# Kernel optimization log

Hardware: AMD Instinct MI355X
Metric: run time of the kernel (lower is better)

The kernel has to match this reference:

```python
import jax, jax.numpy as jnp
import numpy as np

N_NODES = 100000
N_EDGES = 3200000
D_FEAT = 128
HIDDEN = 16
N_CLASSES = 8


def setup_inputs() -> dict:
    key = jax.random.key(0)
    k1, k2, k3, k4 = jax.random.split(key, 4)
    x = jax.random.normal(k1, (N_NODES, D_FEAT), dtype=jnp.float32)
    edge_index = jax.random.randint(k2, (2, N_EDGES), 0, N_NODES, dtype=jnp.int64)
    W1 = jax.random.normal(k3, (D_FEAT, HIDDEN), dtype=jnp.float32) * (1.0 / np.sqrt(D_FEAT))
    b1 = jnp.zeros((HIDDEN,), dtype=jnp.float32)
    W2 = jax.random.normal(k4, (HIDDEN, N_CLASSES), dtype=jnp.float32) * (1.0 / np.sqrt(HIDDEN))
    b2 = jnp.zeros((N_CLASSES,), dtype=jnp.float32)
    return {"x": x, "edge_index": edge_index, "W1": W1, "b1": b1, "W2": W2, "b2": b2}


def _gcn_conv(x, W, b, src, dst, deg_inv_sqrt, n_nodes):
    h = x @ W  # [N, F_out]
    norm = deg_inv_sqrt[src] * deg_inv_sqrt[dst]  # [E']
    msg = h[src] * norm[:, None]  # gather + scale
    out = jax.ops.segment_sum(msg, dst, num_segments=n_nodes)  # scatter-add
    return out + b


def _prep_edges(edge_index, n_nodes):
    # add self-loops (PyG GCNConv default) and compute symmetric norm degrees
    loop = jnp.arange(n_nodes, dtype=edge_index.dtype)
    src = jnp.concatenate([edge_index[0], loop])
    dst = jnp.concatenate([edge_index[1], loop])
    deg = jax.ops.segment_sum(jnp.ones_like(dst, dtype=jnp.float32), dst,
                              num_segments=n_nodes)
    deg_inv_sqrt = jnp.where(deg > 0, jax.lax.rsqrt(jnp.maximum(deg, 1.0)), 0.0)
    return src, dst, deg_inv_sqrt


def reference(x, edge_index, W1, b1, W2, b2):
    n_nodes = x.shape[0]
    src, dst, deg_inv_sqrt = _prep_edges(edge_index, n_nodes)
    h = jax.nn.relu(_gcn_conv(x, W1, b1, src, dst, deg_inv_sqrt, n_nodes))
    logits = _gcn_conv(h, W2, b2, src, dst, deg_inv_sqrt, n_nodes)
    return jax.nn.log_softmax(logits, axis=1)
```

## Files before the change

### kernel.cpp

```cpp
#include <hip/hip_runtime.h>

#define N_NODES 100000
#define N_EDGES 3200000
#define D_FEAT 128
#define HIDDEN 16
#define NCLS 8

#define NBKT 256
#define BSZ  391
#define CHUNK 8192
#define NCHUNK 391
#define TOTH (NBKT * NCHUNK)
#define NBS1 (TOTH / 256)


__global__ __launch_bounds__(256) void k_hist(const int* __restrict__ dst,
                                              unsigned* __restrict__ hist) {
    __shared__ unsigned h[NBKT];
    int tid = threadIdx.x;
    h[tid] = 0u;
    __syncthreads();
    int base = blockIdx.x * CHUNK;
    #pragma unroll
    for (int it = 0; it < CHUNK / 256; ++it) {
        int e = base + it * 256 + tid;
        if (e < N_EDGES) atomicAdd(&h[dst[e] / BSZ], 1u);
    }
    __syncthreads();
    hist[(unsigned)tid * NCHUNK + blockIdx.x] = h[tid];
}

__global__ void k_scan1(unsigned* __restrict__ a, unsigned* __restrict__ bsum) {
    __shared__ unsigned s[256];
    int tid = threadIdx.x;
    int i = blockIdx.x * 256 + tid;
    unsigned v = a[i];
    s[tid] = v; __syncthreads();
    for (int off = 1; off < 256; off <<= 1) {
        unsigned t = (tid >= off) ? s[tid - off] : 0u;
        __syncthreads();
        s[tid] += t;
        __syncthreads();
    }
    a[i] = s[tid] - v;
    if (tid == 255) bsum[blockIdx.x] = s[255];
}

__global__ void k_scan2(unsigned* __restrict__ bsum) {
    __shared__ unsigned s[512];
    int tid = threadIdx.x;
    unsigned v = (tid < NBS1) ? bsum[tid] : 0u;
    s[tid] = v; __syncthreads();
    for (int off = 1; off < 512; off <<= 1) {
        unsigned t = (tid >= off) ? s[tid - off] : 0u;
        __syncthreads();
        s[tid] += t;
        __syncthreads();
    }
    bsum[tid] = s[tid] - v;
}

__global__ void k_scan3(unsigned* __restrict__ a, const unsigned* __restrict__ bsum) {
    int i = blockIdx.x * blockDim.x + threadIdx.x;
    a[i] += bsum[i >> 8];
}

__global__ __launch_bounds__(256) void k_fill(const int* __restrict__ src,
                                              const int* __restrict__ dst,
                                              const unsigned* __restrict__ hist,
                                              unsigned* __restrict__ rec) {
    __shared__ unsigned cur[NBKT];
    int tid = threadIdx.x;
    cur[tid] = hist[(unsigned)tid * NCHUNK + blockIdx.x];
    __syncthreads();
    int base = blockIdx.x * CHUNK;
    #pragma unroll
    for (int it = 0; it < CHUNK / 256; ++it) {
        int e = base + it * 256 + tid;
        if (e < N_EDGES) {
            int d = dst[e];
            int b = d / BSZ;
            unsigned p = atomicAdd(&cur[b], 1u);
            rec[p] = ((unsigned)src[e] << 9) | (unsigned)(d - b * BSZ);
        }
    }
}

__global__ __launch_bounds__(1024) void k_dis2(const unsigned* __restrict__ hist,
                                               const unsigned* __restrict__ rec,
                                               float* __restrict__ dis) {
    __shared__ unsigned cnt[BSZ];
    int tid = threadIdx.x;
    int bkt = blockIdx.x;
    int node0 = bkt * BSZ;
    int nn = (node0 + BSZ <= N_NODES) ? BSZ : (N_NODES - node0);
    for (int n = tid; n < nn; n += 1024) cnt[n] = 1u;
    __syncthreads();
    unsigned start = hist[(unsigned)bkt * NCHUNK];
    unsigned end = (bkt == NBKT - 1) ? N_EDGES : hist[(unsigned)(bkt + 1) * NCHUNK];
    for (unsigned e = start + tid; e < end; e += 1024)
        atomicAdd(&cnt[rec[e] & 511u], 1u);
    __syncthreads();
    for (int n = tid; n < nn; n += 1024)
        dis[node0 + n] = rsqrtf((float)cnt[n]);
}

__global__ __launch_bounds__(256) void k_gemm1(const float* __restrict__ x,
                                               const float* __restrict__ W1,
                                               const float* __restrict__ dis,
                                               float* __restrict__ hd1) {
    __shared__ float sW[D_FEAT * HIDDEN];
    __shared__ float sx[64][132];
    int tid = threadIdx.x;
    for (int t = tid; t < D_FEAT * HIDDEN; t += 256) sW[t] = W1[t];

    int node0 = blockIdx.x * 64;
    #pragma unroll
    for (int it = 0; it < 8; ++it) {
        int lin = it * 256 + tid;
        int r   = lin >> 5;
        int c4  = lin & 31;
        int row = node0 + r;
        float4 v = make_float4(0.f, 0.f, 0.f, 0.f);
        if (row < N_NODES)
            v = *(const float4*)(x + (size_t)row * D_FEAT + c4 * 4);
        *(float4*)(&sx[r][c4 * 4]) = v;
    }
    __syncthreads();

    int lr   = tid >> 2;
    int node = node0 + lr;
    int f0   = (tid & 3) * 4;
    if (node >= N_NODES) return;

    float a0 = 0.f, a1 = 0.f, a2 = 0.f, a3 = 0.f;
    #pragma unroll
    for (int k = 0; k < D_FEAT; ++k) {
        float xv = sx[lr][k];
        a0 += xv * sW[k * HIDDEN + f0 + 0];
        a1 += xv * sW[k * HIDDEN + f0 + 1];
        a2 += xv * sW[k * HIDDEN + f0 + 2];
        a3 += xv * sW[k * HIDDEN + f0 + 3];
    }
    float s = dis[node];
    *(float4*)(hd1 + (size_t)node * HIDDEN + f0) = make_float4(a0 * s, a1 * s, a2 * s, a3 * s);
}

__global__ __launch_bounds__(1024) void k_aggB(const unsigned* __restrict__ hist,
                                               const unsigned* __restrict__ rec,
                                               const float* __restrict__ hd1,
                                               const float* __restrict__ dis,
                                               const float* __restrict__ b1,
                                               const float* __restrict__ W2,
                                               float* __restrict__ hd2) {
    __shared__ float acc[BSZ][HIDDEN + 1];
    __shared__ float sW2[HIDDEN * NCLS];
    __shared__ float sb1[HIDDEN];
    int tid = threadIdx.x;
    int bkt = blockIdx.x;
    int node0 = bkt * BSZ;
    int nn = (node0 + BSZ <= N_NODES) ? BSZ : (N_NODES - node0);
    if (tid < HIDDEN * NCLS) sW2[tid] = W2[tid];
    if (tid < HIDDEN)        sb1[tid] = b1[tid];

    int j = tid & 15, rr = tid >> 4;
    for (int r = rr; r < nn; r += 64)
        acc[r][j] = hd1[(size_t)(node0 + r) * HIDDEN + j];
    __syncthreads();

    unsigned start = hist[(unsigned)bkt * NCHUNK];
    unsigned end = (bkt == NBKT - 1) ? N_EDGES : hist[(unsigned)(bkt + 1) * NCHUNK];
    for (unsigned e = start + rr; e < end; e += 64) {
        unsigned r = rec[e];
        unsigned s = r >> 9, dl = r & 511u;
        float v = hd1[(size_t)s * HIDDEN + j];
        atomicAdd(&acc[dl][j], v);
    }
    __syncthreads();

    for (int n = tid; n < nn; n += 1024) {
        int node = node0 + n;
        float dv = dis[node];
        float hbuf[HIDDEN];
        #pragma unroll
        for (int m = 0; m < HIDDEN; ++m)
            hbuf[m] = fmaxf(dv * acc[n][m] + sb1[m], 0.f);
        float o[NCLS];
        #pragma unroll
        for (int k = 0; k < NCLS; ++k) {
            float t = 0.f;
            #pragma unroll
            for (int m = 0; m < HIDDEN; ++m) t += hbuf[m] * sW2[m * NCLS + k];
            o[k] = dv * t;
        }
        float4* hp = (float4*)(hd2 + (size_t)node * NCLS);
        hp[0] = make_float4(o[0], o[1], o[2], o[3]);
        hp[1] = make_float4(o[4], o[5], o[6], o[7]);
    }
}

__global__ __launch_bounds__(1024) void k_aggC(const unsigned* __restrict__ hist,
                                               const unsigned* __restrict__ rec,
                                               const float* __restrict__ hd2,
                                               const float* __restrict__ dis,
                                               const float* __restrict__ b2,
                                               float* __restrict__ out) {
    __shared__ float acc[BSZ][NCLS + 1];
    int tid = threadIdx.x;
    int bkt = blockIdx.x;
    int node0 = bkt * BSZ;
    int nn = (node0 + BSZ <= N_NODES) ? BSZ : (N_NODES - node0);

    int j = tid & 7, rr = tid >> 3;
    for (int r = rr; r < nn; r += 128)
        acc[r][j] = hd2[(size_t)(node0 + r) * NCLS + j];
    __syncthreads();

    unsigned start = hist[(unsigned)bkt * NCHUNK];
    unsigned end = (bkt == NBKT - 1) ? N_EDGES : hist[(unsigned)(bkt + 1) * NCHUNK];
    for (unsigned e = start + rr; e < end; e += 128) {
        unsigned r = rec[e];
        unsigned s = r >> 9, dl = r & 511u;
        atomicAdd(&acc[dl][j], hd2[(size_t)s * NCLS + j]);
    }
    __syncthreads();

    for (int n = tid; n < nn; n += 1024) {
        int node = node0 + n;
        float dv = dis[node];
        float l[NCLS];
        float m = -1e30f;
        #pragma unroll
        for (int k = 0; k < NCLS; ++k) {
            l[k] = dv * acc[n][k] + b2[k];
            m = fmaxf(m, l[k]);
        }
        float ssum = 0.f;
        #pragma unroll
        for (int k = 0; k < NCLS; ++k) ssum += __expf(l[k] - m);
        float lse = logf(ssum) + m;
        float4* op = (float4*)(out + (size_t)node * NCLS);
        op[0] = make_float4(l[0] - lse, l[1] - lse, l[2] - lse, l[3] - lse);
        op[1] = make_float4(l[4] - lse, l[5] - lse, l[6] - lse, l[7] - lse);
    }
}

extern "C" void kernel_launch(void* const* d_in, const int* in_sizes, int n_in,
                              void* d_out, int out_size, void* d_ws, size_t ws_size,
                              hipStream_t stream) {
    const float* x  = (const float*)d_in[0];
    const int*   ei = (const int*)d_in[1];
    const float* W1 = (const float*)d_in[2];
    const float* b1 = (const float*)d_in[3];
    const float* W2 = (const float*)d_in[4];
    const float* b2 = (const float*)d_in[5];
    float* out = (float*)d_out;

    const int* src = ei;
    const int* dst = ei + N_EDGES;

    unsigned* ws = (unsigned*)d_ws;
    const size_t N = N_NODES;
    float*    dis  = (float*)ws;
    unsigned* hist = ws + N;
    unsigned* bsum = hist + TOTH;
    unsigned* rec  = bsum + 512;
    float*    hd1  = (float*)(rec + N_EDGES);
    float*    hd2  = hd1 + 16 * N;

    k_hist <<<NCHUNK, 256, 0, stream>>>(dst, hist);
    k_scan1<<<NBS1, 256, 0, stream>>>(hist, bsum);
    k_scan2<<<1, 512, 0, stream>>>(bsum);
    k_scan3<<<NBS1, 256, 0, stream>>>(hist, bsum);
    k_fill <<<NCHUNK, 256, 0, stream>>>(src, dst, hist, rec);
    k_dis2 <<<NBKT, 1024, 0, stream>>>(hist, rec, dis);
    k_gemm1<<<(N_NODES + 63) / 64, 256, 0, stream>>>(x, W1, dis, hd1);
    k_aggB <<<NBKT, 1024, 0, stream>>>(hist, rec, hd1, dis, b1, W2, hd2);
    k_aggC <<<NBKT, 1024, 0, stream>>>(hist, rec, hd2, dis, b2, out);
}
```

Before: 597.9 us.

## Split buckets finer and slice edges across blocks with global atomic merge

Doubles the bucket count to 512 with smaller buckets and splits each bucket's edge range across four 256-thread blocks, giving 2048 blocks instead of 256 to raise occupancy on the many CUs. Each slice accumulates partial sums in shared memory and merges them into global buffers with atomics. The per-node epilogues (ReLU plus second GEMM, and log_softmax) become separate node-parallel kernels, and the gather loops are unrolled by four to keep more loads in flight. The cost is extra kernel launches, global atomic traffic, additional buffer writes, and float summation order that is no longer deterministic.

```diff
diff --git a/kernel.cpp b/kernel.cpp
--- a/kernel.cpp
+++ b/kernel.cpp
@@ -6,19 +6,25 @@
 #define HIDDEN 16
 #define NCLS 8
 
-#define NBKT 256
-#define BSZ  391
+#define NBKT 512
+#define BSZ  196
+#define NSLICE 4
 #define CHUNK 8192
 #define NCHUNK 391
 #define TOTH (NBKT * NCHUNK)
 #define NBS1 (TOTH / 256)
 
 
+__global__ void k_zero_deg(unsigned* __restrict__ deg) {
+    int i = blockIdx.x * blockDim.x + threadIdx.x;
+    if (i < N_NODES) deg[i] = 0u;
+}
+
 __global__ __launch_bounds__(256) void k_hist(const int* __restrict__ dst,
                                               unsigned* __restrict__ hist) {
     __shared__ unsigned h[NBKT];
     int tid = threadIdx.x;
-    h[tid] = 0u;
+    h[tid] = 0u; h[tid + 256] = 0u;
     __syncthreads();
     int base = blockIdx.x * CHUNK;
     #pragma unroll
@@ -28,6 +34,7 @@
     }
     __syncthreads();
     hist[(unsigned)tid * NCHUNK + blockIdx.x] = h[tid];
+    hist[(unsigned)(tid + 256) * NCHUNK + blockIdx.x] = h[tid + 256];
 }
 
 __global__ void k_scan1(unsigned* __restrict__ a, unsigned* __restrict__ bsum) {
@@ -47,11 +54,11 @@
 }
 
 __global__ void k_scan2(unsigned* __restrict__ bsum) {
-    __shared__ unsigned s[512];
+    __shared__ unsigned s[1024];
     int tid = threadIdx.x;
     unsigned v = (tid < NBS1) ? bsum[tid] : 0u;
     s[tid] = v; __syncthreads();
-    for (int off = 1; off < 512; off <<= 1) {
+    for (int off = 1; off < 1024; off <<= 1) {
         unsigned t = (tid >= off) ? s[tid - off] : 0u;
         __syncthreads();
         s[tid] += t;
@@ -71,7 +78,8 @@
                                               unsigned* __restrict__ rec) {
     __shared__ unsigned cur[NBKT];
     int tid = threadIdx.x;
-    cur[tid] = hist[(unsigned)tid * NCHUNK + blockIdx.x];
+    cur[tid]       = hist[(unsigned)tid * NCHUNK + blockIdx.x];
+    cur[tid + 256] = hist[(unsigned)(tid + 256) * NCHUNK + blockIdx.x];
     __syncthreads();
     int base = blockIdx.x * CHUNK;
     #pragma unroll
@@ -81,34 +89,41 @@
             int d = dst[e];
             int b = d / BSZ;
             unsigned p = atomicAdd(&cur[b], 1u);
-            rec[p] = ((unsigned)src[e] << 9) | (unsigned)(d - b * BSZ);
+            rec[p] = ((unsigned)src[e] << 8) | (unsigned)(d - b * BSZ);
         }
     }
 }
 
-__global__ __launch_bounds__(1024) void k_dis2(const unsigned* __restrict__ hist,
-                                               const unsigned* __restrict__ rec,
-                                               float* __restrict__ dis) {
+__global__ __launch_bounds__(256) void k_deg(const unsigned* __restrict__ hist,
+                                             const unsigned* __restrict__ rec,
+                                             unsigned* __restrict__ deg) {
     __shared__ unsigned cnt[BSZ];
     int tid = threadIdx.x;
-    int bkt = blockIdx.x;
+    int bkt = blockIdx.x >> 2, slice = blockIdx.x & 3;
     int node0 = bkt * BSZ;
-    int nn = (node0 + BSZ <= N_NODES) ? BSZ : (N_NODES - node0);
-    for (int n = tid; n < nn; n += 1024) cnt[n] = 1u;
+    int nn = N_NODES - node0; if (nn > BSZ) nn = BSZ;
+    if (nn <= 0) return;
+    for (int n = tid; n < nn; n += 256) cnt[n] = 0u;
     __syncthreads();
     unsigned start = hist[(unsigned)bkt * NCHUNK];
     unsigned end = (bkt == NBKT - 1) ? N_EDGES : hist[(unsigned)(bkt + 1) * NCHUNK];
-    for (unsigned e = start + tid; e < end; e += 1024)
-        atomicAdd(&cnt[rec[e] & 511u], 1u);
-    __syncthreads();
-    for (int n = tid; n < nn; n += 1024)
-        dis[node0 + n] = rsqrtf((float)cnt[n]);
+    for (unsigned e = start + slice * 256 + tid; e < end; e += 1024)
+        atomicAdd(&cnt[rec[e] & 255u], 1u);
+    __syncthreads();
+    for (int n = tid; n < nn; n += 256)
+        if (cnt[n]) atomicAdd(&deg[node0 + n], cnt[n]);
+}
+
+__global__ void k_disk(const unsigned* __restrict__ deg, float* __restrict__ dis) {
+    int i = blockIdx.x * blockDim.x + threadIdx.x;
+    if (i < N_NODES) dis[i] = rsqrtf((float)(deg[i] + 1u));
 }
 
 __global__ __launch_bounds__(256) void k_gemm1(const float* __restrict__ x,
                                                const float* __restrict__ W1,
                                                const float* __restrict__ dis,
-                                               float* __restrict__ hd1) {
+                                               float* __restrict__ hd1,
+                                               float* __restrict__ agg1) {
     __shared__ float sW[D_FEAT * HIDDEN];
     __shared__ float sx[64][132];
     int tid = threadIdx.x;
@@ -143,106 +158,153 @@
         a3 += xv * sW[k * HIDDEN + f0 + 3];
     }
     float s = dis[node];
-    *(float4*)(hd1 + (size_t)node * HIDDEN + f0) = make_float4(a0 * s, a1 * s, a2 * s, a3 * s);
-}
-
-__global__ __launch_bounds__(1024) void k_aggB(const unsigned* __restrict__ hist,
-                                               const unsigned* __restrict__ rec,
-                                               const float* __restrict__ hd1,
-                                               const float* __restrict__ dis,
-                                               const float* __restrict__ b1,
-                                               const float* __restrict__ W2,
-                                               float* __restrict__ hd2) {
+    float4 o = make_float4(a0 * s, a1 * s, a2 * s, a3 * s);
+    *(float4*)(hd1  + (size_t)node * HIDDEN + f0) = o;
+    *(float4*)(agg1 + (size_t)node * HIDDEN + f0) = o;
+}
+
+__global__ __launch_bounds__(256) void k_agg1(const unsigned* __restrict__ hist,
+                                              const unsigned* __restrict__ rec,
+                                              const float* __restrict__ hd1,
+                                              float* __restrict__ agg1) {
     __shared__ float acc[BSZ][HIDDEN + 1];
+    int tid = threadIdx.x;
+    int bkt = blockIdx.x >> 2, slice = blockIdx.x & 3;
+    int node0 = bkt * BSZ;
+    int nn = N_NODES - node0; if (nn > BSZ) nn = BSZ;
+    if (nn <= 0) return;
+    for (int t = tid; t < nn * HIDDEN; t += 256) acc[t >> 4][t & 15] = 0.f;
+    __syncthreads();
+
+    unsigned start = hist[(unsigned)bkt * NCHUNK];
+    unsigned end = (bkt == NBKT - 1) ? N_EDGES : hist[(unsigned)(bkt + 1) * NCHUNK];
+    int j = tid & 15, rr = tid >> 4;
+    unsigned e = start + (unsigned)(slice * 16 + rr);
+    for (; e + 192u < end; e += 256u) {
+        unsigned r0 = rec[e], r1 = rec[e + 64u], r2 = rec[e + 128u], r3 = rec[e + 192u];
+        float v0 = hd1[(size_t)(r0 >> 8) * HIDDEN + j];
+        float v1 = hd1[(size_t)(r1 >> 8) * HIDDEN + j];
+        float v2 = hd1[(size_t)(r2 >> 8) * HIDDEN + j];
+        float v3 = hd1[(size_t)(r3 >> 8) * HIDDEN + j];
+        atomicAdd(&acc[r0 & 255u][j], v0);
+        atomicAdd(&acc[r1 & 255u][j], v1);
+        atomicAdd(&acc[r2 & 255u][j], v2);
+        atomicAdd(&acc[r3 & 255u][j], v3);
+    }
+    for (; e < end; e += 64u) {
+        unsigned r = rec[e];
+        atomicAdd(&acc[r & 255u][j], hd1[(size_t)(r >> 8) * HIDDEN + j]);
+    }
+    __syncthreads();
+    for (int t = tid; t < nn * HIDDEN; t += 256) {
+        float v = acc[t >> 4][t & 15];
+        if (v != 0.f) atomicAdd(&agg1[(size_t)node0 * HIDDEN + t], v);
+    }
+}
+
+__global__ __launch_bounds__(256) void k_epi1(const float* __restrict__ agg1,
+                                              const float* __restrict__ dis,
+                                              const float* __restrict__ b1,
+                                              const float* __restrict__ W2,
+                                              float* __restrict__ hd2,
+                                              float* __restrict__ agg2) {
     __shared__ float sW2[HIDDEN * NCLS];
     __shared__ float sb1[HIDDEN];
     int tid = threadIdx.x;
-    int bkt = blockIdx.x;
-    int node0 = bkt * BSZ;
-    int nn = (node0 + BSZ <= N_NODES) ? BSZ : (N_NODES - node0);
     if (tid < HIDDEN * NCLS) sW2[tid] = W2[tid];
     if (tid < HIDDEN)        sb1[tid] = b1[tid];
-
-    int j = tid & 15, rr = tid >> 4;
-    for (int r = rr; r < nn; r += 64)
-        acc[r][j] = hd1[(size_t)(node0 + r) * HIDDEN + j];
+    __syncthreads();
+    int i = blockIdx.x * 256 + tid;
+    if (i >= N_NODES) return;
+    float dv = dis[i];
+    float h[HIDDEN];
+    const float4* ap = (const float4*)(agg1 + (size_t)i * HIDDEN);
+    #pragma unroll
+    for (int q = 0; q < 4; ++q) {
+        float4 a = ap[q];
+        h[q * 4 + 0] = fmaxf(dv * a.x + sb1[q * 4 + 0], 0.f);
+        h[q * 4 + 1] = fmaxf(dv * a.y + sb1[q * 4 + 1], 0.f);
+        h[q * 4 + 2] = fmaxf(dv * a.z + sb1[q * 4 + 2], 0.f);
+        h[q * 4 + 3] = fmaxf(dv * a.w + sb1[q * 4 + 3], 0.f);
+    }
+    float o[NCLS];
+    #pragma unroll
+    for (int k = 0; k < NCLS; ++k) o[k] = 0.f;
+    #pragma unroll
+    for (int m = 0; m < HIDDEN; ++m) {
+        float hv = h[m];
+        #pragma unroll
+        for (int k = 0; k < NCLS; ++k) o[k] += hv * sW2[m * NCLS + k];
+    }
+    float4 o0 = make_float4(dv * o[0], dv * o[1], dv * o[2], dv * o[3]);
+    float4 o1 = make_float4(dv * o[4], dv * o[5], dv * o[6], dv * o[7]);
+    ((float4*)(hd2  + (size_t)i * NCLS))[0] = o0;
+    ((float4*)(hd2  + (size_t)i * NCLS))[1] = o1;
+    ((float4*)(agg2 + (size_t)i * NCLS))[0] = o0;
+    ((float4*)(agg2 + (size_t)i * NCLS))[1] = o1;
+}
+
+__global__ __launch_bounds__(256) void k_agg2(const unsigned* __restrict__ hist,
+                                              const unsigned* __restrict__ rec,
+                                              const float* __restrict__ hd2,
+                                              float* __restrict__ agg2) {
+    __shared__ float acc[BSZ][NCLS + 1];
+    int tid = threadIdx.x;
+    int bkt = blockIdx.x >> 2, slice = blockIdx.x & 3;
+    int node0 = bkt * BSZ;
+    int nn = N_NODES - node0; if (nn > BSZ) nn = BSZ;
+    if (nn <= 0) return;
+    for (int t = tid; t < nn * NCLS; t += 256) acc[t >> 3][t & 7] = 0.f;
     __syncthreads();
 
     unsigned start = hist[(unsigned)bkt * NCHUNK];
     unsigned end = (bkt == NBKT - 1) ? N_EDGES : hist[(unsigned)(bkt + 1) * NCHUNK];
-    for (unsigned e = start + rr; e < end; e += 64) {
+    int j = tid & 7, rr = tid >> 3;
+    unsigned e = start + (unsigned)(slice * 32 + rr);
+    for (; e + 384u < end; e += 512u) {
+        unsigned r0 = rec[e], r1 = rec[e + 128u], r2 = rec[e + 256u], r3 = rec[e + 384u];
+        float v0 = hd2[(size_t)(r0 >> 8) * NCLS + j];
+        float v1 = hd2[(size_t)(r1 >> 8) * NCLS + j];
+        float v2 = hd2[(size_t)(r2 >> 8) * NCLS + j];
+        float v3 = hd2[(size_t)(r3 >> 8) * NCLS + j];
+        atomicAdd(&acc[r0 & 255u][j], v0);
+        atomicAdd(&acc[r1 & 255u][j], v1);
+        atomicAdd(&acc[r2 & 255u][j], v2);
+        atomicAdd(&acc[r3 & 255u][j], v3);
+    }
+    for (; e < end; e += 128u) {
         unsigned r = rec[e];
-        unsigned s = r >> 9, dl = r & 511u;
-        float v = hd1[(size_t)s * HIDDEN + j];
-        atomicAdd(&acc[dl][j], v);
-    }
-    __syncthreads();
-
-    for (int n = tid; n < nn; n += 1024) {
-        int node = node0 + n;
-        float dv = dis[node];
-        float hbuf[HIDDEN];
-        #pragma unroll
-        for (int m = 0; m < HIDDEN; ++m)
-            hbuf[m] = fmaxf(dv * acc[n][m] + sb1[m], 0.f);
-        float o[NCLS];
-        #pragma unroll
-        for (int k = 0; k < NCLS; ++k) {
-            float t = 0.f;
-            #pragma unroll
-            for (int m = 0; m < HIDDEN; ++m) t += hbuf[m] * sW2[m * NCLS + k];
-            o[k] = dv * t;
-        }
-        float4* hp = (float4*)(hd2 + (size_t)node * NCLS);
-        hp[0] = make_float4(o[0], o[1], o[2], o[3]);
-        hp[1] = make_float4(o[4], o[5], o[6], o[7]);
-    }
-}
-
-__global__ __launch_bounds__(1024) void k_aggC(const unsigned* __restrict__ hist,
-                                               const unsigned* __restrict__ rec,
-                                               const float* __restrict__ hd2,
-                                               const float* __restrict__ dis,
-                                               const float* __restrict__ b2,
-                                               float* __restrict__ out) {
-    __shared__ float acc[BSZ][NCLS + 1];
-    int tid = threadIdx.x;
-    int bkt = blockIdx.x;
-    int node0 = bkt * BSZ;
-    int nn = (node0 + BSZ <= N_NODES) ? BSZ : (N_NODES - node0);
-
-    int j = tid & 7, rr = tid >> 3;
-    for (int r = rr; r < nn; r += 128)
-        acc[r][j] = hd2[(size_t)(node0 + r) * NCLS + j];
-    __syncthreads();
-
-    unsigned start = hist[(unsigned)bkt * NCHUNK];
-    unsigned end = (bkt == NBKT - 1) ? N_EDGES : hist[(unsigned)(bkt + 1) * NCHUNK];
-    for (unsigned e = start + rr; e < end; e += 128) {
-        unsigned r = rec[e];
-        unsigned s = r >> 9, dl = r & 511u;
-        atomicAdd(&acc[dl][j], hd2[(size_t)s * NCLS + j]);
-    }
-    __syncthreads();
-
-    for (int n = tid; n < nn; n += 1024) {
-        int node = node0 + n;
-        float dv = dis[node];
-        float l[NCLS];
-        float m = -1e30f;
-        #pragma unroll
-        for (int k = 0; k < NCLS; ++k) {
-            l[k] = dv * acc[n][k] + b2[k];
-            m = fmaxf(m, l[k]);
-        }
-        float ssum = 0.f;
-        #pragma unroll
-        for (int k = 0; k < NCLS; ++k) ssum += __expf(l[k] - m);
-        float lse = logf(ssum) + m;
-        float4* op = (float4*)(out + (size_t)node * NCLS);
-        op[0] = make_float4(l[0] - lse, l[1] - lse, l[2] - lse, l[3] - lse);
-        op[1] = make_float4(l[4] - lse, l[5] - lse, l[6] - lse, l[7] - lse);
-    }
+        atomicAdd(&acc[r & 255u][j], hd2[(size_t)(r >> 8) * NCLS + j]);
+    }
+    __syncthreads();
+    for (int t = tid; t < nn * NCLS; t += 256) {
+        float v = acc[t >> 3][t & 7];
+        if (v != 0.f) atomicAdd(&agg2[(size_t)node0 * NCLS + t], v);
+    }
+}
+
+__global__ void k_epi2(const float* __restrict__ agg2, const float* __restrict__ dis,
+                       const float* __restrict__ b2, float* __restrict__ out) {
+    int i = blockIdx.x * blockDim.x + threadIdx.x;
+    if (i >= N_NODES) return;
+    float dv = dis[i];
+    const float4* ap = (const float4*)(agg2 + (size_t)i * NCLS);
+    float4 a0 = ap[0], a1 = ap[1];
+    float l[NCLS];
+    l[0] = dv * a0.x + b2[0]; l[1] = dv * a0.y + b2[1];
+    l[2] = dv * a0.z + b2[2]; l[3] = dv * a0.w + b2[3];
+    l[4] = dv * a1.x + b2[4]; l[5] = dv * a1.y + b2[5];
+    l[6] = dv * a1.z + b2[6]; l[7] = dv * a1.w + b2[7];
+    float m = l[0];
+    #pragma unroll
+    for (int k = 1; k < NCLS; ++k) m = fmaxf(m, l[k]);
+    float ssum = 0.f;
+    #pragma unroll
+    for (int k = 0; k < NCLS; ++k) ssum += __expf(l[k] - m);
+    float lse = logf(ssum) + m;
+    float4* op = (float4*)(out + (size_t)i * NCLS);
+    op[0] = make_float4(l[0] - lse, l[1] - lse, l[2] - lse, l[3] - lse);
+    op[1] = make_float4(l[4] - lse, l[5] - lse, l[6] - lse, l[7] - lse);
 }
 
 extern "C" void kernel_launch(void* const* d_in, const int* in_sizes, int n_in,
@@ -261,20 +323,29 @@
 
     unsigned* ws = (unsigned*)d_ws;
     const size_t N = N_NODES;
-    float*    dis  = (float*)ws;
-    unsigned* hist = ws + N;
+    unsigned* deg  = ws;
+    float*    dis  = (float*)(ws + N);
+    unsigned* hist = ws + 2 * N;
     unsigned* bsum = hist + TOTH;
-    unsigned* rec  = bsum + 512;
+    unsigned* rec  = bsum + 1024;
     float*    hd1  = (float*)(rec + N_EDGES);
-    float*    hd2  = hd1 + 16 * N;
-
+    float*    agg1 = hd1 + 16 * N;
+    float*    hd2  = agg1 + 16 * N;
+    float*    agg2 = hd2 + 8 * N;
+
+    int nbN = (N_NODES + 255) / 256;
+
+    k_zero_deg<<<nbN, 256, 0, stream>>>(deg);
     k_hist <<<NCHUNK, 256, 0, stream>>>(dst, hist);
     k_scan1<<<NBS1, 256, 0, stream>>>(hist, bsum);
-    k_scan2<<<1, 512, 0, stream>>>(bsum);
+    k_scan2<<<1, 1024, 0, stream>>>(bsum);
     k_scan3<<<NBS1, 256, 0, stream>>>(hist, bsum);
     k_fill <<<NCHUNK, 256, 0, stream>>>(src, dst, hist, rec);
-    k_dis2 <<<NBKT, 1024, 0, stream>>>(hist, rec, dis);
-    k_gemm1<<<(N_NODES + 63) / 64, 256, 0, stream>>>(x, W1, dis, hd1);
-    k_aggB <<<NBKT, 1024, 0, stream>>>(hist, rec, hd1, dis, b1, W2, hd2);
-    k_aggC <<<NBKT, 1024, 0, stream>>>(hist, rec, hd2, dis, b2, out);
-}
+    k_deg  <<<NBKT * NSLICE, 256, 0, stream>>>(hist, rec, deg);
+    k_disk <<<nbN, 256, 0, stream>>>(deg, dis);
+    k_gemm1<<<(N_NODES + 63) / 64, 256, 0, stream>>>(x, W1, dis, hd1, agg1);
+    k_agg1 <<<NBKT * NSLICE, 256, 0, stream>>>(hist, rec, hd1, agg1);
+    k_epi1 <<<nbN, 256, 0, stream>>>(agg1, dis, b1, W2, hd2, agg2);
+    k_agg2 <<<NBKT * NSLICE, 256, 0, stream>>>(hist, rec, hd2, agg2);
+    k_epi2 <<<nbN, 256, 0, stream>>>(agg2, dis, b2, out);
+}
```

After: 576.0 us. 3.7% less time.
